# Kernel tuning notes

Hardware: AMD Instinct MI355X
Metric: run time of the kernel (lower is better)

The kernel has to match this reference:

```python
import jax, jax.numpy as jnp
import numpy as np

N0, N1, N2 = 200000, 100000, 50000
E0, E1 = 1600000, 800000
D_IN, H, C, K = 256, 256, 7, 40  # in_feats, n_hidden, center_num, n_classes


def setup_inputs() -> dict:
    key = jax.random.key(0)
    ks = jax.random.split(key, 11)
    s = 0.05
    inputs = jax.random.normal(ks[0], (N0, D_IN), jnp.float32)
    edge_src0 = jax.random.randint(ks[1], (E0,), 0, N0, jnp.int32)
    edge_dst0 = jax.random.randint(ks[2], (E0,), 0, N1, jnp.int32)
    edge_src1 = jax.random.randint(ks[3], (E1,), 0, N1, jnp.int32)
    edge_dst1 = jax.random.randint(ks[4], (E1,), 0, N2, jnp.int32)
    W_self0 = jax.random.normal(ks[5], (H, D_IN), jnp.float32) * s
    W_neigh0 = jax.random.normal(ks[6], (H, D_IN), jnp.float32) * s
    b0 = jnp.zeros((H,), jnp.float32)
    W_self1 = jax.random.normal(ks[7], (H, H), jnp.float32) * s
    W_neigh1 = jax.random.normal(ks[8], (H, H), jnp.float32) * s
    b1 = jnp.zeros((H,), jnp.float32)
    W_prompt = jax.random.normal(ks[9], (C, 2 * H), jnp.float32) * s
    W_pp = jax.random.normal(ks[10], (C, K, 2 * H), jnp.float32) * s
    return dict(inputs=inputs, W_self0=W_self0, W_neigh0=W_neigh0, b0=b0,
                W_self1=W_self1, W_neigh1=W_neigh1, b1=b1,
                W_prompt=W_prompt, W_pp=W_pp,
                edge_src0=edge_src0, edge_dst0=edge_dst0,
                edge_src1=edge_src1, edge_dst1=edge_dst1)


def _sage_conv(h_src, h_dst, esrc, edst, n_dst, W_self, W_neigh, b):
    # DGL SAGEConv('mean'): fc_self(h_dst) + fc_neigh(mean_{u in N(v)} h_src[u]) + bias
    msg = h_src[esrc]                                            # [E, d]
    summ = jax.ops.segment_sum(msg, edst, num_segments=n_dst)    # [n_dst, d]
    deg = jax.ops.segment_sum(jnp.ones((esrc.shape[0],), msg.dtype), edst,
                              num_segments=n_dst)                # [n_dst]
    mean = summ / jnp.maximum(deg, 1.0)[:, None]
    return h_dst @ W_self.T + mean @ W_neigh.T + b


def _forward(inputs, W_self0, W_neigh0, b0, W_self1, W_neigh1, b1,
             W_prompt, W_pp, edge_src0, edge_dst0, edge_src1, edge_dst1):
    h = inputs  # dropout=0.0 (eval): identity
    # layer 0: N0 src -> N1 dst
    h_dst = h[:N1]
    h = _sage_conv(h, h_dst, edge_src0, edge_dst0, N1, W_self0, W_neigh0, b0)
    h = jax.nn.relu(h)
    # layer 1: N1 src -> N2 dst
    h_dst = h[:N2]
    h = _sage_conv(h, h_dst, edge_src1, edge_dst1, N2, W_self1, W_neigh1, b1)
    h = jax.nn.relu(h)
    neighbor = jax.nn.relu(h_dst)
    hcat = jnp.concatenate([h, neighbor], axis=1)                # [N2, 2H]
    scores = hcat @ W_prompt.T                                   # [N2, C]
    index = jnp.argmax(scores, axis=1)                           # [N2]
    # per-cluster expert Linear, top-1 dispatch/combine
    all_out = jnp.einsum('nd,ckd->nck', hcat, W_pp)              # [N2, C, K]
    out = jnp.take_along_axis(all_out, index[:, None, None], axis=1)[:, 0, :]
    return out


def reference(inputs, W_self0, W_neigh0, b0, W_self1, W_neigh1, b1,
              W_prompt, W_pp, edge_src0, edge_dst0, edge_src1, edge_dst1):
    return _forward(inputs, W_self0, W_neigh0, b0, W_self1, W_neigh1, b1,
                    W_prompt, W_pp, edge_src0, edge_dst0, edge_src1, edge_dst1)
```

## Files before the change

kernel.cpp:

```cpp
#include <hip/hip_runtime.h>
#include <stdint.h>

typedef unsigned short u16;
typedef unsigned int   u32;
typedef short short8 __attribute__((ext_vector_type(8)));
typedef float f32x4  __attribute__((ext_vector_type(4)));
typedef _Float16 f16x4 __attribute__((ext_vector_type(4)));
typedef _Float16 f16x8 __attribute__((ext_vector_type(8)));

#define NN0 200000
#define NN1 100000
#define NN2 50000
#define EE0 1600000
#define EE1 800000
#define DD  256
#define CC  7
#define KK  40

#define ROWW 40
#define LVL_U16 (128 * ROWW)
#define CHUNK_U16 (3 * LVL_U16)

static __device__ __forceinline__ void split3(float x, u32& h0, u32& h1, u32& h2) {
    u32 u = __float_as_uint(x);
    h0 = u & 0xffff0000u;
    float r1 = x - __uint_as_float(h0);
    h1 = __float_as_uint(r1) & 0xffff0000u;
    float r2 = r1 - __uint_as_float(h1);
    h2 = __float_as_uint(r2) & 0xffff0000u;
}

static __device__ __forceinline__ void async16(const void* g, void* l) {
    __builtin_amdgcn_global_load_lds(
        (const __attribute__((address_space(1))) void*)g,
        (__attribute__((address_space(3))) void*)l, 16, 0, 0);
}

__global__ void hist_kernel(const int* __restrict__ dst, int* __restrict__ cnt, int n) {
    int i = blockIdx.x * blockDim.x + threadIdx.x;
    if (i < n) atomicAdd(&cnt[dst[i]], 1);
}

__global__ void scan_block_kernel(const int* __restrict__ in, int* __restrict__ out,
                                  int* __restrict__ partials, int n) {
    __shared__ int sd[256];
    int t = threadIdx.x;
    int base = blockIdx.x * 1024 + t * 4;
    int v0 = (base + 0 < n) ? in[base + 0] : 0;
    int v1 = (base + 1 < n) ? in[base + 1] : 0;
    int v2 = (base + 2 < n) ? in[base + 2] : 0;
    int v3 = (base + 3 < n) ? in[base + 3] : 0;
    int p0 = v0, p1 = p0 + v1, p2 = p1 + v2, p3 = p2 + v3;
    sd[t] = p3;
    __syncthreads();
    for (int off = 1; off < 256; off <<= 1) {
        int x = (t >= off) ? sd[t - off] : 0;
        __syncthreads();
        sd[t] += x;
        __syncthreads();
    }
    int excl = sd[t] - p3;
    if (base + 0 < n) out[base + 0] = excl + p0;
    if (base + 1 < n) out[base + 1] = excl + p1;
    if (base + 2 < n) out[base + 2] = excl + p2;
    if (base + 3 < n) out[base + 3] = excl + p3;
    if (t == 255) partials[blockIdx.x] = sd[255];
}

__global__ void scan_partials_kernel(int* __restrict__ partials, int nb) {
    __shared__ int sd[256];
    int t = threadIdx.x;
    int v = (t < nb) ? partials[t] : 0;
    sd[t] = v;
    __syncthreads();
    for (int off = 1; off < 256; off <<= 1) {
        int x = (t >= off) ? sd[t - off] : 0;
        __syncthreads();
        sd[t] += x;
        __syncthreads();
    }
    if (t < nb) partials[t] = sd[t];
}

__global__ void scan_add_kernel(int* __restrict__ out, const int* __restrict__ partials, int n) {
    int b = blockIdx.x;
    if (b == 0) return;
    int add = partials[b - 1];
    int base = b * 1024 + threadIdx.x * 4;
    if (base + 0 < n) out[base + 0] += add;
    if (base + 1 < n) out[base + 1] += add;
    if (base + 2 < n) out[base + 2] += add;
    if (base + 3 < n) out[base + 3] += add;
}

__global__ void fill_kernel(const int* __restrict__ esrc, const int* __restrict__ edst,
                            const int* __restrict__ rp, int* __restrict__ cur,
                            int* __restrict__ ss, int n) {
    int i = blockIdx.x * blockDim.x + threadIdx.x;
    if (i < n) {
        int d = edst[i];
        int p = rp[d] + atomicAdd(&cur[d], 1);
        ss[p] = esrc[i];
    }
}

__global__ void to_fp16(const float* __restrict__ in, _Float16* __restrict__ outp, long n) {
    long i = ((long)blockIdx.x * blockDim.x + threadIdx.x) * 8;
    if (i >= n) return;
    f32x4 a = *reinterpret_cast<const f32x4*>(in + i);
    f32x4 b = *reinterpret_cast<const f32x4*>(in + i + 4);
    f16x8 h;
    h[0] = (_Float16)a[0]; h[1] = (_Float16)a[1]; h[2] = (_Float16)a[2]; h[3] = (_Float16)a[3];
    h[4] = (_Float16)b[0]; h[5] = (_Float16)b[1]; h[6] = (_Float16)b[2]; h[7] = (_Float16)b[3];
    *reinterpret_cast<f16x8*>(outp + i) = h;
}

__global__ void gather_mean_fp16(const _Float16* __restrict__ Xh, const int* __restrict__ rp,
                                 const int* __restrict__ ss, float* __restrict__ mean, int ndst) {
    int wave = threadIdx.x >> 6, lane = threadIdx.x & 63;
    int d = blockIdx.x * 4 + wave;
    if (d >= ndst) return;
    int beg = rp[d], end = rp[d + 1];
    int lo4 = lane * 4;
    f32x4 a0 = (f32x4)(0.f), a1 = (f32x4)(0.f), a2 = (f32x4)(0.f), a3 = (f32x4)(0.f);
    int j = beg;
    for (; j + 8 <= end; j += 8) {
        int s0 = ss[j + 0], s1 = ss[j + 1], s2 = ss[j + 2], s3 = ss[j + 3];
        int s4 = ss[j + 4], s5 = ss[j + 5], s6 = ss[j + 6], s7 = ss[j + 7];
        f16x4 h0 = *reinterpret_cast<const f16x4*>(Xh + (size_t)s0 * DD + lo4);
        f16x4 h1 = *reinterpret_cast<const f16x4*>(Xh + (size_t)s1 * DD + lo4);
        f16x4 h2 = *reinterpret_cast<const f16x4*>(Xh + (size_t)s2 * DD + lo4);
        f16x4 h3 = *reinterpret_cast<const f16x4*>(Xh + (size_t)s3 * DD + lo4);
        f16x4 h4 = *reinterpret_cast<const f16x4*>(Xh + (size_t)s4 * DD + lo4);
        f16x4 h5 = *reinterpret_cast<const f16x4*>(Xh + (size_t)s5 * DD + lo4);
        f16x4 h6 = *reinterpret_cast<const f16x4*>(Xh + (size_t)s6 * DD + lo4);
        f16x4 h7 = *reinterpret_cast<const f16x4*>(Xh + (size_t)s7 * DD + lo4);
        a0 += __builtin_convertvector(h0, f32x4);
        a1 += __builtin_convertvector(h1, f32x4);
        a2 += __builtin_convertvector(h2, f32x4);
        a3 += __builtin_convertvector(h3, f32x4);
        a0 += __builtin_convertvector(h4, f32x4);
        a1 += __builtin_convertvector(h5, f32x4);
        a2 += __builtin_convertvector(h6, f32x4);
        a3 += __builtin_convertvector(h7, f32x4);
    }
    for (; j + 4 <= end; j += 4) {
        int s0 = ss[j + 0], s1 = ss[j + 1], s2 = ss[j + 2], s3 = ss[j + 3];
        f16x4 h0 = *reinterpret_cast<const f16x4*>(Xh + (size_t)s0 * DD + lo4);
        f16x4 h1 = *reinterpret_cast<const f16x4*>(Xh + (size_t)s1 * DD + lo4);
        f16x4 h2 = *reinterpret_cast<const f16x4*>(Xh + (size_t)s2 * DD + lo4);
        f16x4 h3 = *reinterpret_cast<const f16x4*>(Xh + (size_t)s3 * DD + lo4);
        a0 += __builtin_convertvector(h0, f32x4);
        a1 += __builtin_convertvector(h1, f32x4);
        a2 += __builtin_convertvector(h2, f32x4);
        a3 += __builtin_convertvector(h3, f32x4);
    }
    for (; j < end; ++j) {
        int s = ss[j];
        f16x4 h0 = *reinterpret_cast<const f16x4*>(Xh + (size_t)s * DD + lo4);
        a0 += __builtin_convertvector(h0, f32x4);
    }
    f32x4 s = (a0 + a1) + (a2 + a3);
    int dg = end - beg;
    float inv = 1.0f / (float)(dg > 0 ? dg : 1);
    s *= inv;
    *reinterpret_cast<f32x4*>(mean + (size_t)d * DD + lo4) = s;
}

__global__ void build_wimg(const float* __restrict__ Wa0, const float* __restrict__ Wb0,
                           const float* __restrict__ Wa1, const float* __restrict__ Wb1,
                           u16* __restrict__ img) {
    int blk = blockIdx.x;
    int layer = blk >> 5;
    int ntile = (blk >> 4) & 1;
    int chunk = blk & 15;
    const float* Wa = layer ? Wa1 : Wa0;
    const float* Wb = layer ? Wb1 : Wb0;
    int t = threadIdx.x;
    int row = t >> 1, half = t & 1;
    int n = ntile * 128 + row;
    int kg = chunk * 32 + half * 16;
    const float* W = (kg < 256) ? Wa : Wb;
    int kk = kg & 255;
    const float* src = W + (size_t)n * 256 + kk;
    float x[16];
#pragma unroll
    for (int j = 0; j < 16; j += 4) {
        float4 v = *reinterpret_cast<const float4*>(src + j);
        x[j] = v.x; x[j + 1] = v.y; x[j + 2] = v.z; x[j + 3] = v.w;
    }
    u32 w0[8], w1[8], w2[8];
#pragma unroll
    for (int j = 0; j < 8; ++j) {
        u32 a0, a1, a2, b0, b1, b2;
        split3(x[2 * j], a0, a1, a2);
        split3(x[2 * j + 1], b0, b1, b2);
        w0[j] = (a0 >> 16) | b0; w1[j] = (a1 >> 16) | b1; w2[j] = (a2 >> 16) | b2;
    }
    u16* base = img + (size_t)blk * CHUNK_U16 + row * ROWW + half * 16;
    *reinterpret_cast<uint4*>(base + 0 * LVL_U16)     = make_uint4(w0[0], w0[1], w0[2], w0[3]);
    *reinterpret_cast<uint4*>(base + 0 * LVL_U16 + 8) = make_uint4(w0[4], w0[5], w0[6], w0[7]);
    *reinterpret_cast<uint4*>(base + 1 * LVL_U16)     = make_uint4(w1[0], w1[1], w1[2], w1[3]);
    *reinterpret_cast<uint4*>(base + 1 * LVL_U16 + 8) = make_uint4(w1[4], w1[5], w1[6], w1[7]);
    *reinterpret_cast<uint4*>(base + 2 * LVL_U16)     = make_uint4(w2[0], w2[1], w2[2], w2[3]);
    *reinterpret_cast<uint4*>(base + 2 * LVL_U16 + 8) = make_uint4(w2[4], w2[5], w2[6], w2[7]);
}

__global__ __launch_bounds__(256, 2) void gemm_split(const float* __restrict__ X0,
                                                     const float* __restrict__ X1,
                                                     const u16* __restrict__ imgL,
                                                     const float* __restrict__ bias,
                                                     float* __restrict__ out,
                                                     _Float16* __restrict__ outh, int M) {
    __shared__ __align__(16) u16 Asl[CHUNK_U16];
    __shared__ __align__(16) u16 Bsl[CHUNK_U16];
    int t = threadIdx.x;
    int wave = t >> 6, lane = t & 63;
    int m0 = blockIdx.x * 128;
    int ntile = blockIdx.y;
    int wy = wave >> 1, wx = wave & 1;

    f32x4 acc[4][4];
#pragma unroll
    for (int i = 0; i < 4; ++i)
#pragma unroll
        for (int j = 0; j < 4; ++j) acc[i][j] = (f32x4)(0.f);

    int arow_l = t >> 1;
    int ak = (t & 1) * 16;
    int arow = m0 + arow_l; if (arow >= M) arow = M - 1;

    int frm = wy * 64 + (lane & 15);
    int frn = wx * 64 + (lane & 15);
    int frk = (lane >> 4) * 8;

    const u16* imgT = imgL + (size_t)ntile * 16 * CHUNK_U16;

    for (int c = 0; c < 16; ++c) {
        const u16* src = imgT + (size_t)c * CHUNK_U16;
#pragma unroll
        for (int i = 0; i < 8; ++i) {
            int seg = wave * 8 + i;
            if (seg < 30)
                async16(src + seg * 512 + lane * 8, Bsl + seg * 512 + lane * 8);
        }
        {
            const float* Xs = (c < 8) ? X0 : X1;
            int kc = (c & 7) * 32;
            const float* p = Xs + (size_t)arow * 256 + kc + ak;
            float x[16];
#pragma unroll
            for (int j = 0; j < 16; j += 4) {
                float4 v = *reinterpret_cast<const float4*>(p + j);
                x[j] = v.x; x[j + 1] = v.y; x[j + 2] = v.z; x[j + 3] = v.w;
            }
            u32 w0[8], w1[8], w2[8];
#pragma unroll
            for (int j = 0; j < 8; ++j) {
                u32 a0, a1, a2, b0, b1, b2;
                split3(x[2 * j], a0, a1, a2);
                split3(x[2 * j + 1], b0, b1, b2);
                w0[j] = (a0 >> 16) | b0; w1[j] = (a1 >> 16) | b1; w2[j] = (a2 >> 16) | b2;
            }
            u16* d = Asl + arow_l * ROWW + ak;
            *reinterpret_cast<uint4*>(d + 0 * LVL_U16)     = make_uint4(w0[0], w0[1], w0[2], w0[3]);
            *reinterpret_cast<uint4*>(d + 0 * LVL_U16 + 8) = make_uint4(w0[4], w0[5], w0[6], w0[7]);
            *reinterpret_cast<uint4*>(d + 1 * LVL_U16)     = make_uint4(w1[0], w1[1], w1[2], w1[3]);
            *reinterpret_cast<uint4*>(d + 1 * LVL_U16 + 8) = make_uint4(w1[4], w1[5], w1[6], w1[7]);
            *reinterpret_cast<uint4*>(d + 2 * LVL_U16)     = make_uint4(w2[0], w2[1], w2[2], w2[3]);
            *reinterpret_cast<uint4*>(d + 2 * LVL_U16 + 8) = make_uint4(w2[4], w2[5], w2[6], w2[7]);
        }
        __syncthreads();
        short8 bf[4][3];
#pragma unroll
        for (int ns = 0; ns < 4; ++ns)
#pragma unroll
            for (int l = 0; l < 3; ++l) {
                uint4 v = *reinterpret_cast<const uint4*>(Bsl + l * LVL_U16 + (frn + ns * 16) * ROWW + frk);
                bf[ns][l] = __builtin_bit_cast(short8, v);
            }
#pragma unroll
        for (int ms = 0; ms < 4; ++ms) {
            short8 af[3];
#pragma unroll
            for (int l = 0; l < 3; ++l) {
                uint4 v = *reinterpret_cast<const uint4*>(Asl + l * LVL_U16 + (frm + ms * 16) * ROWW + frk);
                af[l] = __builtin_bit_cast(short8, v);
            }
#pragma unroll
            for (int ns = 0; ns < 4; ++ns) {
                f32x4 a = acc[ms][ns];
                a = __builtin_amdgcn_mfma_f32_16x16x32_bf16(af[0], bf[ns][0], a, 0, 0, 0);
                a = __builtin_amdgcn_mfma_f32_16x16x32_bf16(af[0], bf[ns][1], a, 0, 0, 0);
                a = __builtin_amdgcn_mfma_f32_16x16x32_bf16(af[1], bf[ns][0], a, 0, 0, 0);
                a = __builtin_amdgcn_mfma_f32_16x16x32_bf16(af[0], bf[ns][2], a, 0, 0, 0);
                a = __builtin_amdgcn_mfma_f32_16x16x32_bf16(af[1], bf[ns][1], a, 0, 0, 0);
                a = __builtin_amdgcn_mfma_f32_16x16x32_bf16(af[2], bf[ns][0], a, 0, 0, 0);
                acc[ms][ns] = a;
            }
        }
        __syncthreads();
    }
#pragma unroll
    for (int ms = 0; ms < 4; ++ms) {
        int rbase = m0 + wy * 64 + ms * 16 + (lane >> 4) * 4;
#pragma unroll
        for (int ns = 0; ns < 4; ++ns) {
            int col = ntile * 128 + wx * 64 + ns * 16 + (lane & 15);
            float bcol = bias[col];
#pragma unroll
            for (int r = 0; r < 4; ++r) {
                int row = rbase + r;
                if (row < M) {
                    float v = fmaxf(acc[ms][ns][r] + bcol, 0.f);
                    out[(size_t)row * DD + col] = v;
                    if (outh) outh[(size_t)row * DD + col] = (_Float16)v;
                }
            }
        }
    }
}

__global__ void final_kernel(const float* __restrict__ h2, const float* __restrict__ h1,
                             const float* __restrict__ Wp, const float* __restrict__ Wpp,
                             float* __restrict__ out) {
    int wave = threadIdx.x >> 6, lane = threadIdx.x & 63;
    int nd = blockIdx.x * 4 + wave;
    if (nd >= NN2) return;
    int d0 = lane * 8;
    const float* src = (d0 < 256) ? (h2 + (size_t)nd * DD + d0)
                                  : (h1 + (size_t)nd * DD + (d0 - 256));
    float4 v0 = *reinterpret_cast<const float4*>(src);
    float4 v1 = *reinterpret_cast<const float4*>(src + 4);
    float x[8] = {v0.x, v0.y, v0.z, v0.w, v1.x, v1.y, v1.z, v1.w};

    float best = -3.0e38f; int bc = 0;
#pragma unroll
    for (int c = 0; c < CC; ++c) {
        const float* w = Wp + (size_t)c * 512 + d0;
        float4 w0 = *reinterpret_cast<const float4*>(w);
        float4 w1 = *reinterpret_cast<const float4*>(w + 4);
        float p = x[0] * w0.x + x[1] * w0.y + x[2] * w0.z + x[3] * w0.w
                + x[4] * w1.x + x[5] * w1.y + x[6] * w1.z + x[7] * w1.w;
        p += __shfl_xor(p, 32); p += __shfl_xor(p, 16); p += __shfl_xor(p, 8);
        p += __shfl_xor(p, 4);  p += __shfl_xor(p, 2);  p += __shfl_xor(p, 1);
        if (p > best) { best = p; bc = c; }
    }
    for (int k = 0; k < KK; ++k) {
        const float* w = Wpp + ((size_t)bc * KK + k) * 512 + d0;
        float4 w0 = *reinterpret_cast<const float4*>(w);
        float4 w1 = *reinterpret_cast<const float4*>(w + 4);
        float p = x[0] * w0.x + x[1] * w0.y + x[2] * w0.z + x[3] * w0.w
                + x[4] * w1.x + x[5] * w1.y + x[6] * w1.z + x[7] * w1.w;
        p += __shfl_xor(p, 32); p += __shfl_xor(p, 16); p += __shfl_xor(p, 8);
        p += __shfl_xor(p, 4);  p += __shfl_xor(p, 2);  p += __shfl_xor(p, 1);
        if (lane == 0) out[(size_t)nd * KK + k] = p;
    }
}

extern "C" void kernel_launch(void* const* d_in, const int* in_sizes, int n_in,
                              void* d_out, int out_size, void* d_ws, size_t ws_size,
                              hipStream_t stream) {
    const float* inputs  = (const float*)d_in[0];
    const float* Wself0  = (const float*)d_in[1];
    const float* Wneigh0 = (const float*)d_in[2];
    const float* b0      = (const float*)d_in[3];
    const float* Wself1  = (const float*)d_in[4];
    const float* Wneigh1 = (const float*)d_in[5];
    const float* b1      = (const float*)d_in[6];
    const float* Wp      = (const float*)d_in[7];
    const float* Wpp     = (const float*)d_in[8];
    const int* es0 = (const int*)d_in[9];
    const int* ed0 = (const int*)d_in[10];
    const int* es1 = (const int*)d_in[11];
    const int* ed1 = (const int*)d_in[12];

    char* ws = (char*)d_ws;
    size_t off = 0;
    auto alloc = [&](size_t bytes) -> void* {
        void* p = (void*)(ws + off);
        off += (bytes + 255) & ~(size_t)255;
        return p;
    };
    int* cnt0 = (int*)alloc((size_t)NN1 * 4);
    int* cnt1 = (int*)alloc((size_t)NN2 * 4);
    int* cur0 = (int*)alloc((size_t)NN1 * 4);
    int* cur1 = (int*)alloc((size_t)NN2 * 4);
    int* rp0  = (int*)alloc((size_t)(NN1 + 1) * 4);
    int* rp1  = (int*)alloc((size_t)(NN2 + 1) * 4);
    int* part0 = (int*)alloc(1024);
    int* part1 = (int*)alloc(1024);
    size_t zero_bytes = off;
    int*   ss0   = (int*)alloc((size_t)EE0 * 4);
    int*   ss1   = (int*)alloc((size_t)EE1 * 4);
    u16*   wimg  = (u16*)alloc((size_t)64 * CHUNK_U16 * 2);
    _Float16* xh = (_Float16*)alloc((size_t)NN0 * DD * 2);
    float*    h1 = (float*)xh;
    _Float16* h1h  = (_Float16*)alloc((size_t)NN1 * DD * 2);
    float* mean0 = (float*)alloc((size_t)NN1 * DD * 4);
    float* mean1 = mean0;
    float* h2    = mean0 + (size_t)NN2 * DD;

    hipMemsetAsync(d_ws, 0, zero_bytes, stream);

    hist_kernel<<<(EE0 + 255) / 256, 256, 0, stream>>>(ed0, cnt0, EE0);
    hist_kernel<<<(EE1 + 255) / 256, 256, 0, stream>>>(ed1, cnt1, EE1);
    int nb0 = (NN1 + 1023) / 1024, nb1 = (NN2 + 1023) / 1024;
    scan_block_kernel<<<nb0, 256, 0, stream>>>(cnt0, rp0 + 1, part0, NN1);
    scan_partials_kernel<<<1, 256, 0, stream>>>(part0, nb0);
    scan_add_kernel<<<nb0, 256, 0, stream>>>(rp0 + 1, part0, NN1);
    scan_block_kernel<<<nb1, 256, 0, stream>>>(cnt1, rp1 + 1, part1, NN2);
    scan_partials_kernel<<<1, 256, 0, stream>>>(part1, nb1);
    scan_add_kernel<<<nb1, 256, 0, stream>>>(rp1 + 1, part1, NN2);
    fill_kernel<<<(EE0 + 255) / 256, 256, 0, stream>>>(es0, ed0, rp0, cur0, ss0, EE0);
    fill_kernel<<<(EE1 + 255) / 256, 256, 0, stream>>>(es1, ed1, rp1, cur1, ss1, EE1);

    build_wimg<<<64, 256, 0, stream>>>(Wself0, Wneigh0, Wself1, Wneigh1, wimg);

    long nx = (long)NN0 * DD;
    to_fp16<<<(int)(nx / 8 / 256), 256, 0, stream>>>(inputs, xh, nx);

    gather_mean_fp16<<<(NN1 + 3) / 4, 256, 0, stream>>>(xh, rp0, ss0, mean0, NN1);
    dim3 g0((NN1 + 127) / 128, 2);
    gemm_split<<<g0, 256, 0, stream>>>(inputs, mean0, wimg, b0, h1, h1h, NN1);

    gather_mean_fp16<<<(NN2 + 3) / 4, 256, 0, stream>>>(h1h, rp1, ss1, mean1, NN2);
    dim3 g1((NN2 + 127) / 128, 2);
    gemm_split<<<g1, 256, 0, stream>>>(h1, mean1, wimg + (size_t)32 * CHUNK_U16, b1, h2, nullptr, NN2);

    final_kernel<<<(NN2 + 3) / 4, 256, 0, stream>>>(h2, h1, Wp, Wpp, (float*)d_out);
}
```

Measured before the change: 1.225 ms.

## Replace 3-way bf16 split GEMM with 2-way fp16 split and XOR-swizzled LDS

Switches the error-compensated GEMM from a three-term bf16 decomposition (six MFMAs per tile step) to a two-term fp16 hi/lo split (three MFMAs per step). The weight image and LDS tiles move from a padded row stride of 40 to a dense 32-wide layout with an XOR swizzle that avoids bank conflicts. The smaller LDS footprint allows a launch bound of 3 blocks per SM instead of 2. The risks are reduced precision, since fp16 has less exponent range than bf16 and residuals may underflow or overflow, and possible accuracy-tolerance failures.

```diff
diff --git a/kernel.cpp b/kernel.cpp
--- a/kernel.cpp
+++ b/kernel.cpp
@@ -3,7 +3,6 @@
 
 typedef unsigned short u16;
 typedef unsigned int   u32;
-typedef short short8 __attribute__((ext_vector_type(8)));
 typedef float f32x4  __attribute__((ext_vector_type(4)));
 typedef _Float16 f16x4 __attribute__((ext_vector_type(4)));
 typedef _Float16 f16x8 __attribute__((ext_vector_type(8)));
@@ -17,17 +16,19 @@
 #define CC  7
 #define KK  40
 
-#define ROWW 40
-#define LVL_U16 (128 * ROWW)
-#define CHUNK_U16 (3 * LVL_U16)
-
-static __device__ __forceinline__ void split3(float x, u32& h0, u32& h1, u32& h2) {
-    u32 u = __float_as_uint(x);
-    h0 = u & 0xffff0000u;
-    float r1 = x - __uint_as_float(h0);
-    h1 = __float_as_uint(r1) & 0xffff0000u;
-    float r2 = r1 - __uint_as_float(h1);
-    h2 = __float_as_uint(r2) & 0xffff0000u;
+#define LVL2_U16 4096
+#define IMG_U16  8192
+
+static __device__ __forceinline__ void split2(float x, _Float16& t0, _Float16& t1) {
+    t0 = (_Float16)x;
+    t1 = (_Float16)(x - (float)t0);
+}
+
+static __device__ __forceinline__ f16x8 pack8(const _Float16* h) {
+    f16x8 v;
+#pragma unroll
+    for (int i = 0; i < 8; ++i) v[i] = h[i];
+    return v;
 }
 
 static __device__ __forceinline__ void async16(const void* g, void* l) {
@@ -189,31 +190,27 @@
         float4 v = *reinterpret_cast<const float4*>(src + j);
         x[j] = v.x; x[j + 1] = v.y; x[j + 2] = v.z; x[j + 3] = v.w;
     }
-    u32 w0[8], w1[8], w2[8];
-#pragma unroll
-    for (int j = 0; j < 8; ++j) {
-        u32 a0, a1, a2, b0, b1, b2;
-        split3(x[2 * j], a0, a1, a2);
-        split3(x[2 * j + 1], b0, b1, b2);
-        w0[j] = (a0 >> 16) | b0; w1[j] = (a1 >> 16) | b1; w2[j] = (a2 >> 16) | b2;
-    }
-    u16* base = img + (size_t)blk * CHUNK_U16 + row * ROWW + half * 16;
-    *reinterpret_cast<uint4*>(base + 0 * LVL_U16)     = make_uint4(w0[0], w0[1], w0[2], w0[3]);
-    *reinterpret_cast<uint4*>(base + 0 * LVL_U16 + 8) = make_uint4(w0[4], w0[5], w0[6], w0[7]);
-    *reinterpret_cast<uint4*>(base + 1 * LVL_U16)     = make_uint4(w1[0], w1[1], w1[2], w1[3]);
-    *reinterpret_cast<uint4*>(base + 1 * LVL_U16 + 8) = make_uint4(w1[4], w1[5], w1[6], w1[7]);
-    *reinterpret_cast<uint4*>(base + 2 * LVL_U16)     = make_uint4(w2[0], w2[1], w2[2], w2[3]);
-    *reinterpret_cast<uint4*>(base + 2 * LVL_U16 + 8) = make_uint4(w2[4], w2[5], w2[6], w2[7]);
-}
-
-__global__ __launch_bounds__(256, 2) void gemm_split(const float* __restrict__ X0,
-                                                     const float* __restrict__ X1,
-                                                     const u16* __restrict__ imgL,
-                                                     const float* __restrict__ bias,
-                                                     float* __restrict__ out,
-                                                     _Float16* __restrict__ outh, int M) {
-    __shared__ __align__(16) u16 Asl[CHUNK_U16];
-    __shared__ __align__(16) u16 Bsl[CHUNK_U16];
+    _Float16 h0[16], h1[16];
+#pragma unroll
+    for (int j = 0; j < 16; ++j) split2(x[j], h0[j], h1[j]);
+    int rs = (row >> 1) & 3;
+    int q0 = (half * 2 + 0) ^ rs;
+    int q1 = (half * 2 + 1) ^ rs;
+    u16* base = img + (size_t)blk * IMG_U16 + row * 32;
+    *reinterpret_cast<f16x8*>(base + q0 * 8)            = pack8(h0);
+    *reinterpret_cast<f16x8*>(base + q1 * 8)            = pack8(h0 + 8);
+    *reinterpret_cast<f16x8*>(base + LVL2_U16 + q0 * 8) = pack8(h1);
+    *reinterpret_cast<f16x8*>(base + LVL2_U16 + q1 * 8) = pack8(h1 + 8);
+}
+
+__global__ __launch_bounds__(256, 3) void gemm_f16(const float* __restrict__ X0,
+                                                   const float* __restrict__ X1,
+                                                   const u16* __restrict__ imgL,
+                                                   const float* __restrict__ bias,
+                                                   float* __restrict__ out,
+                                                   _Float16* __restrict__ outh, int M) {
+    __shared__ __align__(16) u16 Asl[2 * LVL2_U16];
+    __shared__ __align__(16) u16 Bsl[2 * LVL2_U16];
     int t = threadIdx.x;
     int wave = t >> 6, lane = t & 63;
     int m0 = blockIdx.x * 128;
@@ -227,75 +224,66 @@
         for (int j = 0; j < 4; ++j) acc[i][j] = (f32x4)(0.f);
 
     int arow_l = t >> 1;
-    int ak = (t & 1) * 16;
+    int akh = t & 1;
     int arow = m0 + arow_l; if (arow >= M) arow = M - 1;
 
-    int frm = wy * 64 + (lane & 15);
-    int frn = wx * 64 + (lane & 15);
-    int frk = (lane >> 4) * 8;
-
-    const u16* imgT = imgL + (size_t)ntile * 16 * CHUNK_U16;
+    int fr = lane & 15;
+    int q  = lane >> 4;
+    int frm = wy * 64 + fr;
+    int frn = wx * 64 + fr;
+
+    const u16* imgT = imgL + (size_t)ntile * 16 * IMG_U16;
 
     for (int c = 0; c < 16; ++c) {
-        const u16* src = imgT + (size_t)c * CHUNK_U16;
-#pragma unroll
-        for (int i = 0; i < 8; ++i) {
-            int seg = wave * 8 + i;
-            if (seg < 30)
-                async16(src + seg * 512 + lane * 8, Bsl + seg * 512 + lane * 8);
+        const char* src = (const char*)(imgT + (size_t)c * IMG_U16);
+#pragma unroll
+        for (int i = 0; i < 4; ++i) {
+            int seg = wave * 4 + i;
+            async16(src + seg * 1024 + lane * 16, (char*)Bsl + seg * 1024 + lane * 16);
         }
         {
             const float* Xs = (c < 8) ? X0 : X1;
             int kc = (c & 7) * 32;
-            const float* p = Xs + (size_t)arow * 256 + kc + ak;
+            const float* p = Xs + (size_t)arow * 256 + kc + akh * 16;
             float x[16];
 #pragma unroll
             for (int j = 0; j < 16; j += 4) {
                 float4 v = *reinterpret_cast<const float4*>(p + j);
                 x[j] = v.x; x[j + 1] = v.y; x[j + 2] = v.z; x[j + 3] = v.w;
             }
-            u32 w0[8], w1[8], w2[8];
-#pragma unroll
-            for (int j = 0; j < 8; ++j) {
-                u32 a0, a1, a2, b0, b1, b2;
-                split3(x[2 * j], a0, a1, a2);
-                split3(x[2 * j + 1], b0, b1, b2);
-                w0[j] = (a0 >> 16) | b0; w1[j] = (a1 >> 16) | b1; w2[j] = (a2 >> 16) | b2;
-            }
-            u16* d = Asl + arow_l * ROWW + ak;
-            *reinterpret_cast<uint4*>(d + 0 * LVL_U16)     = make_uint4(w0[0], w0[1], w0[2], w0[3]);
-            *reinterpret_cast<uint4*>(d + 0 * LVL_U16 + 8) = make_uint4(w0[4], w0[5], w0[6], w0[7]);
-            *reinterpret_cast<uint4*>(d + 1 * LVL_U16)     = make_uint4(w1[0], w1[1], w1[2], w1[3]);
-            *reinterpret_cast<uint4*>(d + 1 * LVL_U16 + 8) = make_uint4(w1[4], w1[5], w1[6], w1[7]);
-            *reinterpret_cast<uint4*>(d + 2 * LVL_U16)     = make_uint4(w2[0], w2[1], w2[2], w2[3]);
-            *reinterpret_cast<uint4*>(d + 2 * LVL_U16 + 8) = make_uint4(w2[4], w2[5], w2[6], w2[7]);
+            _Float16 h0[16], h1[16];
+#pragma unroll
+            for (int j = 0; j < 16; ++j) split2(x[j], h0[j], h1[j]);
+            int rs = (arow_l >> 1) & 3;
+            int q0 = (akh * 2 + 0) ^ rs;
+            int q1 = (akh * 2 + 1) ^ rs;
+            u16* d = Asl + arow_l * 32;
+            *reinterpret_cast<f16x8*>(d + q0 * 8)            = pack8(h0);
+            *reinterpret_cast<f16x8*>(d + q1 * 8)            = pack8(h0 + 8);
+            *reinterpret_cast<f16x8*>(d + LVL2_U16 + q0 * 8) = pack8(h1);
+            *reinterpret_cast<f16x8*>(d + LVL2_U16 + q1 * 8) = pack8(h1 + 8);
         }
         __syncthreads();
-        short8 bf[4][3];
-#pragma unroll
-        for (int ns = 0; ns < 4; ++ns)
-#pragma unroll
-            for (int l = 0; l < 3; ++l) {
-                uint4 v = *reinterpret_cast<const uint4*>(Bsl + l * LVL_U16 + (frn + ns * 16) * ROWW + frk);
-                bf[ns][l] = __builtin_bit_cast(short8, v);
-            }
+        f16x8 bf[4][2];
+#pragma unroll
+        for (int ns = 0; ns < 4; ++ns) {
+            int r = frn + ns * 16;
+            int off = r * 32 + ((q ^ ((r >> 1) & 3))) * 8;
+            bf[ns][0] = *reinterpret_cast<const f16x8*>(Bsl + off);
+            bf[ns][1] = *reinterpret_cast<const f16x8*>(Bsl + LVL2_U16 + off);
+        }
 #pragma unroll
         for (int ms = 0; ms < 4; ++ms) {
-            short8 af[3];
-#pragma unroll
-            for (int l = 0; l < 3; ++l) {
-                uint4 v = *reinterpret_cast<const uint4*>(Asl + l * LVL_U16 + (frm + ms * 16) * ROWW + frk);
-                af[l] = __builtin_bit_cast(short8, v);
-            }
+            int r = frm + ms * 16;
+            int off = r * 32 + ((q ^ ((r >> 1) & 3))) * 8;
+            f16x8 af0 = *reinterpret_cast<const f16x8*>(Asl + off);
+            f16x8 af1 = *reinterpret_cast<const f16x8*>(Asl + LVL2_U16 + off);
 #pragma unroll
             for (int ns = 0; ns < 4; ++ns) {
                 f32x4 a = acc[ms][ns];
-                a = __builtin_amdgcn_mfma_f32_16x16x32_bf16(af[0], bf[ns][0], a, 0, 0, 0);
-                a = __builtin_amdgcn_mfma_f32_16x16x32_bf16(af[0], bf[ns][1], a, 0, 0, 0);
-                a = __builtin_amdgcn_mfma_f32_16x16x32_bf16(af[1], bf[ns][0], a, 0, 0, 0);
-                a = __builtin_amdgcn_mfma_f32_16x16x32_bf16(af[0], bf[ns][2], a, 0, 0, 0);
-                a = __builtin_amdgcn_mfma_f32_16x16x32_bf16(af[1], bf[ns][1], a, 0, 0, 0);
-                a = __builtin_amdgcn_mfma_f32_16x16x32_bf16(af[2], bf[ns][0], a, 0, 0, 0);
+                a = __builtin_amdgcn_mfma_f32_16x16x32_f16(af0, bf[ns][0], a, 0, 0, 0);
+                a = __builtin_amdgcn_mfma_f32_16x16x32_f16(af0, bf[ns][1], a, 0, 0, 0);
+                a = __builtin_amdgcn_mfma_f32_16x16x32_f16(af1, bf[ns][0], a, 0, 0, 0);
                 acc[ms][ns] = a;
             }
         }
@@ -393,7 +381,7 @@
     size_t zero_bytes = off;
     int*   ss0   = (int*)alloc((size_t)EE0 * 4);
     int*   ss1   = (int*)alloc((size_t)EE1 * 4);
-    u16*   wimg  = (u16*)alloc((size_t)64 * CHUNK_U16 * 2);
+    u16*   wimg  = (u16*)alloc((size_t)64 * IMG_U16 * 2);
     _Float16* xh = (_Float16*)alloc((size_t)NN0 * DD * 2);
     float*    h1 = (float*)xh;
     _Float16* h1h  = (_Float16*)alloc((size_t)NN1 * DD * 2);
@@ -422,11 +410,11 @@
 
     gather_mean_fp16<<<(NN1 + 3) / 4, 256, 0, stream>>>(xh, rp0, ss0, mean0, NN1);
     dim3 g0((NN1 + 127) / 128, 2);
-    gemm_split<<<g0, 256, 0, stream>>>(inputs, mean0, wimg, b0, h1, h1h, NN1);
+    gemm_f16<<<g0, 256, 0, stream>>>(inputs, mean0, wimg, b0, h1, h1h, NN1);
 
     gather_mean_fp16<<<(NN2 + 3) / 4, 256, 0, stream>>>(h1h, rp1, ss1, mean1, NN2);
     dim3 g1((NN2 + 127) / 128, 2);
-    gemm_split<<<g1, 256, 0, stream>>>(h1, mean1, wimg + (size_t)32 * CHUNK_U16, b1, h2, nullptr, NN2);
+    gemm_f16<<<g1, 256, 0, stream>>>(h1, mean1, wimg + (size_t)32 * IMG_U16, b1, h2, nullptr, NN2);
 
     final_kernel<<<(NN2 + 3) / 4, 256, 0, stream>>>(h2, h1, Wp, Wpp, (float*)d_out);
 }
```

Result: faster. 1.114 ms (-9.0%).
